# Performance work log

Measured on AMD Instinct MI355X. Metric: run time of the kernel, lower is better.

## Reference

```python
import jax, jax.numpy as jnp
import numpy as np

NUM_HEADS = 16
HEAD_DIM = 64
HIDDEN = NUM_HEADS * HEAD_DIM  # 1024


def get_rel_pos(q_size, k_size, rel_pos):
    # q_size == k_size here and rel_pos already has 2*size-1 rows, so the
    # F.interpolate(mode='linear') resize in the original is an identity.
    # relative_coords = q - k + (k_size - 1)  (scale factors are 1.0)
    coords = jnp.arange(q_size)[:, None] - jnp.arange(k_size)[None, :] + (k_size - 1)
    return rel_pos[coords]  # [q_size, k_size, head_dim]


def setup_inputs() -> dict:
    key = jax.random.key(0)
    ks = jax.random.split(key, 7)
    B, H, W = 4, 56, 28
    inp = {
        "hidden_states": jax.random.normal(ks[0], (B, H, W, HIDDEN), jnp.float32),
        "qkv_w": jax.random.normal(ks[1], (3 * HIDDEN, HIDDEN), jnp.float32) * 0.02,
        "qkv_b": jax.random.normal(ks[2], (3 * HIDDEN,), jnp.float32) * 0.02,
        "proj_w": jax.random.normal(ks[3], (HIDDEN, HIDDEN), jnp.float32) * 0.02,
        "proj_b": jax.random.normal(ks[4], (HIDDEN,), jnp.float32) * 0.02,
        "rel_pos_h": jax.random.normal(ks[5], (2 * H - 1, HEAD_DIM), jnp.float32) * 0.02,
        "rel_pos_w": jax.random.normal(ks[6], (2 * W - 1, HEAD_DIM), jnp.float32) * 0.02,
    }
    return inp


def reference(hidden_states, qkv_w, qkv_b, proj_w, proj_b, rel_pos_h, rel_pos_w):
    B, H, W, C = hidden_states.shape
    N = H * W
    scale = HEAD_DIM ** -0.5

    # qkv projection -> [3, B*heads, N, head_dim]
    qkv = hidden_states @ qkv_w.T + qkv_b
    qkv = qkv.reshape(B, N, 3, NUM_HEADS, HEAD_DIM).transpose(2, 0, 3, 1, 4)
    qkv = qkv.reshape(3, B * NUM_HEADS, N, HEAD_DIM)
    query, key_, value = qkv[0], qkv[1], qkv[2]

    # scaled dot-product scores, fully materialized as in the original
    attn = jnp.einsum('bqd,bkd->bqk', query * scale, key_)  # [B*heads, N, N]

    # decomposed relative position bias
    Rh = get_rel_pos(H, H, rel_pos_h)  # [H, H, d]
    Rw = get_rel_pos(W, W, rel_pos_w)  # [W, W, d]
    q_r = query.reshape(B * NUM_HEADS, H, W, HEAD_DIM)
    rel_h = jnp.einsum('bhwc,hkc->bhwk', q_r, Rh)  # [B*heads, H, W, H]
    rel_w = jnp.einsum('bhwc,wkc->bhwk', q_r, Rw)  # [B*heads, H, W, W]
    attn = attn.reshape(B * NUM_HEADS, H, W, H, W)
    attn = attn + rel_h[:, :, :, :, None] + rel_w[:, :, :, None, :]
    attn = attn.reshape(B * NUM_HEADS, N, N)

    attn = jax.nn.softmax(attn.astype(jnp.float32), axis=-1).astype(query.dtype)

    out = jnp.einsum('bqk,bkd->bqd', attn, value)
    out = out.reshape(B, NUM_HEADS, H, W, HEAD_DIM).transpose(0, 2, 3, 1, 4)
    out = out.reshape(B, H, W, C)
    out = out @ proj_w.T + proj_b
    return out
```

## Files before the change

kernel.cpp:

```cpp
#include <hip/hip_runtime.h>
#include <hip/hip_bf16.h>
#include <stdint.h>

typedef __bf16 bf16;
typedef __bf16 bf16x2 __attribute__((ext_vector_type(2)));
typedef __bf16 bf16x4 __attribute__((ext_vector_type(4)));
typedef __bf16 bf16x8 __attribute__((ext_vector_type(8)));
typedef float f32x4 __attribute__((ext_vector_type(4)));

#define AS1 __attribute__((address_space(1)))
#define AS3 __attribute__((address_space(3)))

static __device__ __forceinline__ void async_cp16(const bf16* g, bf16* l) {
    __builtin_amdgcn_global_load_lds((const AS1 void*)g, (AS3 void*)l, 16, 0, 0);
}

static __device__ __forceinline__ bf16x4 cvt4(f32x4 v) {
    bf16x4 r;
    r[0] = (bf16)v[0]; r[1] = (bf16)v[1]; r[2] = (bf16)v[2]; r[3] = (bf16)v[3];
    return r;
}

static __device__ __forceinline__ float fast_exp2(float x) {
#if __has_builtin(__builtin_amdgcn_exp2f)
    return __builtin_amdgcn_exp2f(x);
#else
    return __expf(x * 0.69314718056f);
#endif
}

__global__ __launch_bounds__(256) void cvt_kernel(
    const float* __restrict__ src, bf16* __restrict__ dst, int n4) {
    int i = blockIdx.x * 256 + threadIdx.x;
    const int stride = gridDim.x * 256;
    for (; i < n4; i += stride)
        ((bf16x4*)dst)[i] = cvt4(((const f32x4*)src)[i]);
}

__global__ __launch_bounds__(256) void build_kone(bf16* __restrict__ Kone) {
    const int idx = blockIdx.x * 256 + threadIdx.x;
    if (idx >= 6400) return;
    const int key = idx >> 2, chunk = idx & 3;
    const int hk = key / 28;
    const int wk = key - hk * 28;
    const int kt = key >> 6;
    const int ha = (kt << 6) / 28;
    const int jw = 27 - wk;
    const int jh = 31 - (hk - ha);
    bf16x8 v;
#pragma unroll
    for (int e = 0; e < 8; e++) {
        const int j = chunk * 8 + e;
        v[e] = (j == jw || j == jh) ? (bf16)1.0f : (bf16)0.0f;
    }
    *(bf16x8*)&Kone[key * 32 + chunk * 8] = v;
}

__global__ __launch_bounds__(256) void zero_slack(
    bf16* __restrict__ a, bf16* __restrict__ b) {
    const int i = threadIdx.x;
    bf16x8 z = {};
    *(bf16x8*)&a[i * 8] = z;
    *(bf16x8*)&b[i * 8] = z;
}


#define QKV_EPILOGUE()                                                        \
    for (int nt = 0; nt < 4; nt++) {                                          \
        const int n_ = n0 + wn + nt * 16 + lm;                                \
        const float bv = bias[n_];                                            \
        const int s = n_ >> 10, rem = n_ & 1023;                              \
        const int h = rem >> 6, d = rem & 63;                                 \
        const float qsc = (s == 0) ? 0.18033688011112042f : 1.0f;             \
        for (int mt = 0; mt < 4; mt++) {                                      \
            for (int r = 0; r < 4; r++) {                                     \
                const int m_ = m0 + wm + mt * 16 + quad * 4 + r;              \
                const int b = m_ / 1568;                                      \
                const int pix = m_ - b * 1568;                                \
                const int g = b * 16 + h;                                     \
                const bf16 v = (bf16)((acc[mt][nt][r] + bv) * qsc);           \
                if (s == 0)      Qb[((size_t)g * 1568 + pix) * 64 + d] = v;   \
                else if (s == 1) Kb[((size_t)g * 1568 + pix) * 64 + d] = v;   \
                else {                                                        \
                    const int lk = pix & 31;                                  \
                    const int ppix = (pix & ~31) | ((lk & 15) << 1) | (lk >> 4); \
                    Vt[((size_t)g * 64 + d) * 1568 + ppix] = v;               \
                }                                                             \
            }                                                                 \
        }                                                                     \
    }


__global__ __launch_bounds__(256) void qkv_gemm_bf16(
    const bf16* __restrict__ A, const bf16* __restrict__ W,
    const float* __restrict__ bias, bf16* __restrict__ Qb,
    bf16* __restrict__ Kb, bf16* __restrict__ Vt) {
    __shared__ bf16 As[128 * 32];
    __shared__ bf16 Bs[128 * 32];
    const int t = threadIdx.x;
    const int wid = t >> 6, lane = t & 63;
    const int bid = blockIdx.x;
    const int widx = (bid & 7) * 147 + (bid >> 3);
    const int mt_ = widx / 24;
    const int m0 = mt_ * 128, n0 = (widx - mt_ * 24) * 128;
    const int wm = (wid & 1) * 64, wn = (wid >> 1) * 64;
    const int r_i = lane >> 2, c8 = (lane & 3) * 8;
    const int lm = lane & 15, quad = lane >> 4;

    f32x4 acc[4][4] = {};
    for (int k0 = 0; k0 < 1024; k0 += 32) {
        __syncthreads();
        for (int i = 0; i < 2; i++) {
            const int blk = wid * 2 + i;
            async_cp16(A + (size_t)(m0 + blk * 16 + r_i) * 1024 + k0 + c8, As + blk * 512);
            async_cp16(W + (size_t)(n0 + blk * 16 + r_i) * 1024 + k0 + c8, Bs + blk * 512);
        }
        __syncthreads();
        bf16x8 af[4], bfr[4];
        for (int x = 0; x < 4; x++) {
            af[x]  = *(const bf16x8*)&As[(wm + x * 16 + lm) * 32 + quad * 8];
            bfr[x] = *(const bf16x8*)&Bs[(wn + x * 16 + lm) * 32 + quad * 8];
        }
        for (int mt = 0; mt < 4; mt++)
            for (int nt = 0; nt < 4; nt++)
                acc[mt][nt] = __builtin_amdgcn_mfma_f32_16x16x32_bf16(af[mt], bfr[nt], acc[mt][nt], 0, 0, 0);
    }
    QKV_EPILOGUE()
}

__global__ __launch_bounds__(256) void qkv_gemm_f32(
    const float* __restrict__ A, const float* __restrict__ W,
    const float* __restrict__ bias, bf16* __restrict__ Qb,
    bf16* __restrict__ Kb, bf16* __restrict__ Vt) {
    __shared__ bf16 As[128 * 32];
    __shared__ bf16 Bs[128 * 32];
    const int t = threadIdx.x;
    const int wid = t >> 6, lane = t & 63;
    const int bid = blockIdx.x;
    const int widx = (bid & 7) * 147 + (bid >> 3);
    const int mt_ = widx / 24;
    const int m0 = mt_ * 128, n0 = (widx - mt_ * 24) * 128;
    const int wm = (wid & 1) * 64, wn = (wid >> 1) * 64;
    const int lm = lane & 15, quad = lane >> 4;

    f32x4 acc[4][4] = {};
    for (int k0 = 0; k0 < 1024; k0 += 32) {
        __syncthreads();
        for (int i = 0; i < 4; i++) {
            const int idx = t + i * 256;
            const int row = idx >> 3, c4 = (idx & 7) * 4;
            const f32x4 av = *(const f32x4*)&A[(size_t)(m0 + row) * 1024 + k0 + c4];
            const f32x4 wv = *(const f32x4*)&W[(size_t)(n0 + row) * 1024 + k0 + c4];
            *(bf16x4*)&As[row * 32 + c4] = cvt4(av);
            *(bf16x4*)&Bs[row * 32 + c4] = cvt4(wv);
        }
        __syncthreads();
        bf16x8 af[4], bfr[4];
        for (int x = 0; x < 4; x++) {
            af[x]  = *(const bf16x8*)&As[(wm + x * 16 + lm) * 32 + quad * 8];
            bfr[x] = *(const bf16x8*)&Bs[(wn + x * 16 + lm) * 32 + quad * 8];
        }
        for (int mt = 0; mt < 4; mt++)
            for (int nt = 0; nt < 4; nt++)
                acc[mt][nt] = __builtin_amdgcn_mfma_f32_16x16x32_bf16(af[mt], bfr[nt], acc[mt][nt], 0, 0, 0);
    }
    QKV_EPILOGUE()
}

__global__ __launch_bounds__(256) void flash_attn(
    const bf16* __restrict__ Qb, const bf16* __restrict__ Kb,
    const bf16* __restrict__ Vt, const float* __restrict__ rph,
    const float* __restrict__ rpw, const bf16* __restrict__ Kone,
    bf16* __restrict__ AO) {
    const int x = blockIdx.x;
    const int xcd = x & 7, j = x >> 3;
    const int g = xcd * 8 + j / 25;
    const int qblk = j - (j / 25) * 25;
    const int q0 = qblk * 64;
    const int hqb = q0 / 28;

    __shared__ __align__(16) char smem[51200];
    bf16* Th = (bf16*)smem;
    const char* ThC = (const char*)smem;
    char* B = smem + 8192;
    bf16* Qs  = (bf16*)(B + 32768);
    bf16* RPh = (bf16*)(B + 0);
    bf16* RPw = (bf16*)(B + 9216);
    float* TwF = (float*)(B + 18432);
    bf16* TwS = (bf16*)(B + 33280);

    const int t = threadIdx.x, wid = t >> 6, lane = t & 63;
    const int lm = lane & 15, quad = lane >> 4;
    const int qbase_l = wid * 16 + quad * 4;
    const int swz = (lm & 7) << 4;
    const int l3 = lane >> 3, l7 = lane & 7;
    const int swe = ((l7 ^ l3) << 3);

    const bf16* kSrc[2];
    const bf16* vSrc[2];
#pragma unroll
    for (int i = 0; i < 2; i++) {
        kSrc[i] = Kb + ((size_t)g * 1568 + wid * 16 + i * 8 + l3) * 64 + swe;
        vSrc[i] = Vt + ((size_t)g * 64 + wid * 16 + i * 8 + l3) * 1568 + swe;
    }

    for (int c = t; c < 512; c += 256) {
        const int row = c >> 3, col = (c & 7) * 8;
        const int qg = min(q0 + row, 1567);
        *(bf16x8*)&Qs[row * 72 + col] =
            *(const bf16x8*)&Qb[((size_t)g * 1568 + qg) * 64 + col];
    }
    for (int c = t; c < 1024; c += 256) {
        const int row = c >> 4, col = (c & 15) * 4;
        const int rg = min(hqb + row, 110);
        *(bf16x4*)&RPh[row * 72 + col] = cvt4(*(const f32x4*)&rph[rg * 64 + col]);
    }
    __syncthreads();

    const int qrow_l = wid * 16 + lm;
    const bf16x8 qf0 = *(const bf16x8*)&Qs[qrow_l * 72 + quad * 8];
    const bf16x8 qf1 = *(const bf16x8*)&Qs[qrow_l * 72 + 32 + quad * 8];
    const int qgl = min(q0 + qrow_l, 1567);
    const int thb2 = (qrow_l * 64 + (qgl / 28 - hqb) + 54) * 2;

    for (int c = t; c < 1024; c += 256) {
        const int row = c >> 4, col = (c & 15) * 4;
        const int rg = min(row, 54);
        *(bf16x4*)&RPw[row * 72 + col] = cvt4(*(const f32x4*)&rpw[rg * 64 + col]);
    }
    f32x4 acch[4];
#pragma unroll
    for (int nt = 0; nt < 4; nt++) {
        const bf16x8 b0 = *(const bf16x8*)&RPh[(nt * 16 + lm) * 72 + quad * 8];
        const bf16x8 b1 = *(const bf16x8*)&RPh[(nt * 16 + lm) * 72 + 32 + quad * 8];
        f32x4 a = {};
        a = __builtin_amdgcn_mfma_f32_16x16x32_bf16(qf0, b0, a, 0, 0, 0);
        a = __builtin_amdgcn_mfma_f32_16x16x32_bf16(qf1, b1, a, 0, 0, 0);
        acch[nt] = a;
    }
    __syncthreads();

#pragma unroll
    for (int nt = 0; nt < 4; nt++) {
        const int c = nt * 16 + lm;
        if (c < 59) {
#pragma unroll
            for (int r = 0; r < 4; r++)
                Th[(qbase_l + r) * 64 + c + 2] = (bf16)(acch[nt][r] * 8.0f);
        }
    }
    if (lm == 0) {
#pragma unroll
        for (int r = 0; r < 4; r++) {
            Th[(qbase_l + r) * 64 + 0] = (bf16)0.0f;
            Th[(qbase_l + r) * 64 + 1] = (bf16)0.0f;
        }
    }
#pragma unroll
    for (int nt = 0; nt < 4; nt++) {
        const bf16x8 b0 = *(const bf16x8*)&RPw[(nt * 16 + lm) * 72 + quad * 8];
        const bf16x8 b1 = *(const bf16x8*)&RPw[(nt * 16 + lm) * 72 + 32 + quad * 8];
        f32x4 a = {};
        a = __builtin_amdgcn_mfma_f32_16x16x32_bf16(qf0, b0, a, 0, 0, 0);
        a = __builtin_amdgcn_mfma_f32_16x16x32_bf16(qf1, b1, a, 0, 0, 0);
        const int c = nt * 16 + lm;
        if (c < 55) {
#pragma unroll
            for (int r = 0; r < 4; r++)
                TwF[(qbase_l + r) * 58 + c] = a[r] * 8.0f;
        }
    }
    __syncthreads();

    {
        const int row = t >> 2, chunk = t & 3;
        const int qg = min(q0 + row, 1567);
        const int wq = qg % 28;
        const float* src = &TwF[row * 58 + wq];
        bf16x8 v;
        if (chunk < 3) {
#pragma unroll
            for (int e = 0; e < 8; e++) v[e] = (bf16)src[chunk * 8 + e];
        } else {
#pragma unroll
            for (int e = 0; e < 4; e++) v[e] = (bf16)src[24 + e];
#pragma unroll
            for (int e = 4; e < 8; e++) v[e] = (bf16)0.0f;
        }
        *(bf16x8*)&TwS[row * 32 + chunk * 8] = v;
    }
    __syncthreads();

    const bf16x8 qt_mine = *(const bf16x8*)&TwS[qrow_l * 32 + quad * 8];

#pragma unroll
    for (int i = 0; i < 2; i++) {
        async_cp16(kSrc[i], (bf16*)(B + (wid * 2 + i) * 1024));
        async_cp16(vSrc[i], (bf16*)(B + 16384 + (wid * 2 + i) * 1024));
        kSrc[i] += 4096;
        vSrc[i] += 64;
    }
    const bf16* kop = Kone + lm * 32 + quad * 8;
    bf16x8 ko[4];
#pragma unroll
    for (int f = 0; f < 4; f++) ko[f] = *(const bf16x8*)(kop + f * 512);
    __syncthreads();

    f32x4 o[4] = {};
    f32x4 lsum = {};
    const f32x4 zero4 = {};
    bf16x8 ones;
#pragma unroll
    for (int i = 0; i < 8; i++) ones[i] = (bf16)1.0f;

    bf16* P0w = (bf16*)(B + 32768) + wid * 640;
    bf16* P1w = (bf16*)(B + 37888) + wid * 640;

    int curo = 0;
    for (int kt = 0; kt < 25; kt++) {
        bf16x8 qf2 = qt_mine;
        if (quad == 3) {
            const int ha = (kt << 6) / 28;
            const char* tp = ThC + (thb2 - (ha << 1));
            qf2[4] = *(const bf16*)(tp);
            qf2[5] = *(const bf16*)(tp + 2);
            qf2[6] = *(const bf16*)(tp + 4);
            qf2[7] = *(const bf16*)(tp + 6);
        }

        if (kt < 24) {
            const int nxto = curo ^ 8192;
#pragma unroll
            for (int i = 0; i < 2; i++) {
                async_cp16(kSrc[i], (bf16*)(B + nxto + (wid * 2 + i) * 1024));
                async_cp16(vSrc[i], (bf16*)(B + 16384 + nxto + (wid * 2 + i) * 1024));
                kSrc[i] += 4096;
                vSrc[i] += 64;
            }
        }

        __builtin_amdgcn_s_setprio(1);
        f32x4 s[4];
#pragma unroll
        for (int f = 0; f < 4; f++)
            s[f] = __builtin_amdgcn_mfma_f32_16x16x32_bf16(qf2, ko[f], zero4, 0, 0, 0);
        {
            const char* KsB = B + curo;
            const int x0 = (quad * 16) ^ swz;
#pragma unroll
            for (int f = 0; f < 4; f++) {
                const char* rp = KsB + (f * 16 + lm) * 128;
                const bf16x8 ka = *(const bf16x8*)(rp + x0);
                const bf16x8 kb2 = *(const bf16x8*)(rp + (x0 ^ 64));
                s[f] = __builtin_amdgcn_mfma_f32_16x16x32_bf16(qf0, ka, s[f], 0, 0, 0);
                s[f] = __builtin_amdgcn_mfma_f32_16x16x32_bf16(qf1, kb2, s[f], 0, 0, 0);
            }
        }
        __builtin_amdgcn_s_setprio(0);

        if (kt < 24) {
            kop += 2048;
#pragma unroll
            for (int f = 0; f < 4; f++) ko[f] = *(const bf16x8*)(kop + f * 512);
        }

        if (kt == 24) {
#pragma unroll
            for (int r = 0; r < 4; r++) { s[2][r] = -30000.0f; s[3][r] = -30000.0f; }
        }

#pragma unroll
        for (int r = 0; r < 4; r++) {
            const float a0 = fast_exp2(s[0][r]);
            const float a1 = fast_exp2(s[1][r]);
            bf16x2 pp; pp[0] = (bf16)a0; pp[1] = (bf16)a1;
            *(bf16x2*)&P0w[(quad * 4 + r) * 40 + lm * 2] = pp;
            const float b0 = fast_exp2(s[2][r]);
            const float b1 = fast_exp2(s[3][r]);
            bf16x2 qq; qq[0] = (bf16)b0; qq[1] = (bf16)b1;
            *(bf16x2*)&P1w[(quad * 4 + r) * 40 + lm * 2] = qq;
        }
        __asm__ volatile("s_waitcnt lgkmcnt(0)" ::: "memory");
        const bf16x8 pf0 = *(const bf16x8*)&P0w[lm * 40 + quad * 8];
        const bf16x8 pf1 = *(const bf16x8*)&P1w[lm * 40 + quad * 8];
        lsum = __builtin_amdgcn_mfma_f32_16x16x32_bf16(pf0, ones, lsum, 0, 0, 0);
        lsum = __builtin_amdgcn_mfma_f32_16x16x32_bf16(pf1, ones, lsum, 0, 0, 0);
        __builtin_amdgcn_s_setprio(1);
        {
            const char* VsB = B + 16384 + curo;
#pragma unroll
            for (int dt = 0; dt < 4; dt++) {
                const bf16x8 vf = *(const bf16x8*)(VsB + (dt * 16 + lm) * 128 +
                                                   ((quad * 16) ^ swz));
                o[dt] = __builtin_amdgcn_mfma_f32_16x16x32_bf16(pf0, vf, o[dt], 0, 0, 0);
            }
#pragma unroll
            for (int dt = 0; dt < 4; dt++) {
                const bf16x8 vf = *(const bf16x8*)(VsB + (dt * 16 + lm) * 128 +
                                                   ((64 + quad * 16) ^ swz));
                o[dt] = __builtin_amdgcn_mfma_f32_16x16x32_bf16(pf1, vf, o[dt], 0, 0, 0);
            }
        }
        __builtin_amdgcn_s_setprio(0);

        if (kt < 24) {
            __syncthreads();
            curo ^= 8192;
        }
    }

    if (q0 + wid * 16 < 1568) {
        const int bo = g >> 4, hh = g & 15;
#pragma unroll
        for (int r = 0; r < 4; r++) {
            const float inv = 1.0f / lsum[r];
            const size_t base = ((size_t)bo * 1568 + q0 + qbase_l + r) * 1024 + hh * 64;
#pragma unroll
            for (int dt = 0; dt < 4; dt++)
                AO[base + dt * 16 + lm] = (bf16)(o[dt][r] * inv);
        }
    }
}

__global__ __launch_bounds__(256) void proj_gemm_bf16(
    const bf16* __restrict__ A, const bf16* __restrict__ W,
    const float* __restrict__ bias, float* __restrict__ out) {
    __shared__ bf16 As[128 * 32];
    __shared__ bf16 Bs[128 * 32];
    const int t = threadIdx.x;
    const int wid = t >> 6, lane = t & 63;
    const int bid = blockIdx.x;
    const int widx = (bid & 7) * 49 + (bid >> 3);
    const int m0 = (widx >> 3) * 128, n0 = (widx & 7) * 128;
    const int wm = (wid & 1) * 64, wn = (wid >> 1) * 64;
    const int r_i = lane >> 2, c8 = (lane & 3) * 8;
    const int lm = lane & 15, quad = lane >> 4;

    f32x4 acc[4][4] = {};
    for (int k0 = 0; k0 < 1024; k0 += 32) {
        __syncthreads();
        for (int i = 0; i < 2; i++) {
            const int blk = wid * 2 + i;
            async_cp16(A + (size_t)(m0 + blk * 16 + r_i) * 1024 + k0 + c8, As + blk * 512);
            async_cp16(W + (size_t)(n0 + blk * 16 + r_i) * 1024 + k0 + c8, Bs + blk * 512);
        }
        __syncthreads();
        bf16x8 af[4], bfr[4];
        for (int x = 0; x < 4; x++) {
            af[x]  = *(const bf16x8*)&As[(wm + x * 16 + lm) * 32 + quad * 8];
            bfr[x] = *(const bf16x8*)&Bs[(wn + x * 16 + lm) * 32 + quad * 8];
        }
        for (int mt = 0; mt < 4; mt++)
            for (int nt = 0; nt < 4; nt++)
                acc[mt][nt] = __builtin_amdgcn_mfma_f32_16x16x32_bf16(af[mt], bfr[nt], acc[mt][nt], 0, 0, 0);
    }
    for (int nt = 0; nt < 4; nt++) {
        const int n_ = n0 + wn + nt * 16 + lm;
        const float bv = bias[n_];
        for (int mt = 0; mt < 4; mt++)
            for (int r = 0; r < 4; r++) {
                const int m_ = m0 + wm + mt * 16 + quad * 4 + r;
                out[(size_t)m_ * 1024 + n_] = acc[mt][nt][r] + bv;
            }
    }
}

__global__ __launch_bounds__(256) void proj_gemm_f32(
    const bf16* __restrict__ A, const float* __restrict__ W,
    const float* __restrict__ bias, float* __restrict__ out) {
    __shared__ bf16 As[128 * 32];
    __shared__ bf16 Bs[128 * 32];
    const int t = threadIdx.x;
    const int wid = t >> 6, lane = t & 63;
    const int bid = blockIdx.x;
    const int widx = (bid & 7) * 49 + (bid >> 3);
    const int m0 = (widx >> 3) * 128, n0 = (widx & 7) * 128;
    const int wm = (wid & 1) * 64, wn = (wid >> 1) * 64;
    const int r_i = lane >> 2, c8 = (lane & 3) * 8;
    const int lm = lane & 15, quad = lane >> 4;

    f32x4 acc[4][4] = {};
    for (int k0 = 0; k0 < 1024; k0 += 32) {
        __syncthreads();
        for (int i = 0; i < 2; i++) {
            const int blk = wid * 2 + i;
            async_cp16(A + (size_t)(m0 + blk * 16 + r_i) * 1024 + k0 + c8, As + blk * 512);
        }
        for (int i = 0; i < 4; i++) {
            const int idx = t + i * 256;
            const int row = idx >> 3, c4 = (idx & 7) * 4;
            const f32x4 wv = *(const f32x4*)&W[(size_t)(n0 + row) * 1024 + k0 + c4];
            *(bf16x4*)&Bs[row * 32 + c4] = cvt4(wv);
        }
        __syncthreads();
        bf16x8 af[4], bfr[4];
        for (int x = 0; x < 4; x++) {
            af[x]  = *(const bf16x8*)&As[(wm + x * 16 + lm) * 32 + quad * 8];
            bfr[x] = *(const bf16x8*)&Bs[(wn + x * 16 + lm) * 32 + quad * 8];
        }
        for (int mt = 0; mt < 4; mt++)
            for (int nt = 0; nt < 4; nt++)
                acc[mt][nt] = __builtin_amdgcn_mfma_f32_16x16x32_bf16(af[mt], bfr[nt], acc[mt][nt], 0, 0, 0);
    }
    for (int nt = 0; nt < 4; nt++) {
        const int n_ = n0 + wn + nt * 16 + lm;
        const float bv = bias[n_];
        for (int mt = 0; mt < 4; mt++)
            for (int r = 0; r < 4; r++) {
                const int m_ = m0 + wm + mt * 16 + quad * 4 + r;
                out[(size_t)m_ * 1024 + n_] = acc[mt][nt][r] + bv;
            }
    }
}

extern "C" void kernel_launch(void* const* d_in, const int* in_sizes, int n_in,
                              void* d_out, int out_size, void* d_ws, size_t ws_size,
                              hipStream_t stream) {
    const float* hs     = (const float*)d_in[0];
    const float* qkv_w  = (const float*)d_in[1];
    const float* qkv_b  = (const float*)d_in[2];
    const float* proj_w = (const float*)d_in[3];
    const float* proj_b = (const float*)d_in[4];
    const float* rph    = (const float*)d_in[5];
    const float* rpw    = (const float*)d_in[6];
    float* out = (float*)d_out;

    const size_t GQ  = (size_t)64 * 1568 * 64;
    const size_t SL  = 2048;
    const size_t N_KONE = (size_t)1600 * 32;
    const size_t N_HS = (size_t)6272 * 1024;
    const size_t N_QW = (size_t)3072 * 1024;
    const size_t N_PW = (size_t)1024 * 1024;
    bf16* Qb = (bf16*)d_ws;
    bf16* Kb = Qb + GQ;
    bf16* Vt = Kb + GQ + SL;
    bf16* AO = Vt + GQ + SL;
    bf16* Kone = AO + GQ;
    bf16* hs_bf    = Kone + N_KONE;
    bf16* qkvw_bf  = hs_bf + N_HS;
    bf16* projw_bf = qkvw_bf + N_QW;
    const size_t need = (4 * GQ + 2 * SL + N_KONE + N_HS + N_QW + N_PW) * sizeof(bf16);

    if (ws_size >= need) {
        build_kone<<<25, 256, 0, stream>>>(Kone);
        zero_slack<<<1, 256, 0, stream>>>(Kb + GQ, Vt + GQ);
        cvt_kernel<<<512, 256, 0, stream>>>(hs, hs_bf, (int)(N_HS / 4));
        cvt_kernel<<<512, 256, 0, stream>>>(qkv_w, qkvw_bf, (int)(N_QW / 4));
        cvt_kernel<<<256, 256, 0, stream>>>(proj_w, projw_bf, (int)(N_PW / 4));
        qkv_gemm_bf16<<<1176, 256, 0, stream>>>(hs_bf, qkvw_bf, qkv_b, Qb, Kb, Vt);
        flash_attn<<<1600, 256, 0, stream>>>(Qb, Kb, Vt, rph, rpw, Kone, AO);
        proj_gemm_bf16<<<392, 256, 0, stream>>>(AO, projw_bf, proj_b, out);
    } else {
        build_kone<<<25, 256, 0, stream>>>(Kone);
        zero_slack<<<1, 256, 0, stream>>>(Kb + GQ, Vt + GQ);
        qkv_gemm_f32<<<1176, 256, 0, stream>>>(hs, qkv_w, qkv_b, Qb, Kb, Vt);
        flash_attn<<<1600, 256, 0, stream>>>(Qb, Kb, Vt, rph, rpw, Kone, AO);
        proj_gemm_f32<<<392, 256, 0, stream>>>(AO, proj_w, proj_b, out);
    }
}
```

Before: 310.1 us.

## Double-buffer GEMM LDS tiles and merge setup/convert kernels into fewer launches

The QKV and projection GEMMs now use two LDS buffers. The next K-slice is prefetched while MFMAs run on the current one, which removes one barrier per iteration and hides global load latency. The three fp32-to-bf16 convert launches are merged into one kernel over a contiguous destination, and the Kone build and slack zeroing are merged into another, cutting launch overhead. Doubling LDS per block to 32KB may lower occupancy. Correctness relies on the hs_bf, qkvw_bf and projw_bf buffers being contiguous in the workspace.

```diff
diff --git a/kernel.cpp b/kernel.cpp
--- a/kernel.cpp
+++ b/kernel.cpp
@@ -29,39 +29,46 @@
 #endif
 }
 
-__global__ __launch_bounds__(256) void cvt_kernel(
-    const float* __restrict__ src, bf16* __restrict__ dst, int n4) {
+__global__ __launch_bounds__(256) void cvt_all(
+    const float* __restrict__ hs, const float* __restrict__ qw,
+    const float* __restrict__ pw, bf16* __restrict__ dst) {
+    const int H4 = 6272 * 1024 / 4, Q4 = 3072 * 1024 / 4, P4 = 1024 * 1024 / 4;
+    const int total = H4 + Q4 + P4;
     int i = blockIdx.x * 256 + threadIdx.x;
     const int stride = gridDim.x * 256;
-    for (; i < n4; i += stride)
-        ((bf16x4*)dst)[i] = cvt4(((const f32x4*)src)[i]);
-}
-
-__global__ __launch_bounds__(256) void build_kone(bf16* __restrict__ Kone) {
+    for (; i < total; i += stride) {
+        f32x4 v;
+        if (i < H4)            v = ((const f32x4*)hs)[i];
+        else if (i < H4 + Q4)  v = ((const f32x4*)qw)[i - H4];
+        else                   v = ((const f32x4*)pw)[i - H4 - Q4];
+        ((bf16x4*)dst)[i] = cvt4(v);
+    }
+}
+
+__global__ __launch_bounds__(256) void setup_misc(
+    bf16* __restrict__ Kone, bf16* __restrict__ slackA, bf16* __restrict__ slackB) {
     const int idx = blockIdx.x * 256 + threadIdx.x;
-    if (idx >= 6400) return;
-    const int key = idx >> 2, chunk = idx & 3;
-    const int hk = key / 28;
-    const int wk = key - hk * 28;
-    const int kt = key >> 6;
-    const int ha = (kt << 6) / 28;
-    const int jw = 27 - wk;
-    const int jh = 31 - (hk - ha);
-    bf16x8 v;
-#pragma unroll
-    for (int e = 0; e < 8; e++) {
-        const int j = chunk * 8 + e;
-        v[e] = (j == jw || j == jh) ? (bf16)1.0f : (bf16)0.0f;
-    }
-    *(bf16x8*)&Kone[key * 32 + chunk * 8] = v;
-}
-
-__global__ __launch_bounds__(256) void zero_slack(
-    bf16* __restrict__ a, bf16* __restrict__ b) {
-    const int i = threadIdx.x;
-    bf16x8 z = {};
-    *(bf16x8*)&a[i * 8] = z;
-    *(bf16x8*)&b[i * 8] = z;
+    if (idx < 6400) {
+        const int key = idx >> 2, chunk = idx & 3;
+        const int hk = key / 28;
+        const int wk = key - hk * 28;
+        const int kt = key >> 6;
+        const int ha = (kt << 6) / 28;
+        const int jw = 27 - wk;
+        const int jh = 31 - (hk - ha);
+        bf16x8 v;
+#pragma unroll
+        for (int e = 0; e < 8; e++) {
+            const int j = chunk * 8 + e;
+            v[e] = (j == jw || j == jh) ? (bf16)1.0f : (bf16)0.0f;
+        }
+        *(bf16x8*)&Kone[key * 32 + chunk * 8] = v;
+    } else if (idx < 6656) {
+        const int i = idx - 6400;
+        bf16x8 z = {};
+        *(bf16x8*)&slackA[i * 8] = z;
+        *(bf16x8*)&slackB[i * 8] = z;
+    }
 }
 
 
@@ -95,8 +102,8 @@
     const bf16* __restrict__ A, const bf16* __restrict__ W,
     const float* __restrict__ bias, bf16* __restrict__ Qb,
     bf16* __restrict__ Kb, bf16* __restrict__ Vt) {
-    __shared__ bf16 As[128 * 32];
-    __shared__ bf16 Bs[128 * 32];
+    __shared__ bf16 As[2][128 * 32];
+    __shared__ bf16 Bs[2][128 * 32];
     const int t = threadIdx.x;
     const int wid = t >> 6, lane = t & 63;
     const int bid = blockIdx.x;
@@ -107,24 +114,33 @@
     const int r_i = lane >> 2, c8 = (lane & 3) * 8;
     const int lm = lane & 15, quad = lane >> 4;
 
+#define QKV_STAGE(buf, kk)                                                     \
+    for (int i = 0; i < 2; i++) {                                              \
+        const int blk = wid * 2 + i;                                           \
+        async_cp16(A + (size_t)(m0 + blk * 16 + r_i) * 1024 + (kk) + c8,       \
+                   &As[buf][blk * 512]);                                       \
+        async_cp16(W + (size_t)(n0 + blk * 16 + r_i) * 1024 + (kk) + c8,       \
+                   &Bs[buf][blk * 512]);                                       \
+    }
+
     f32x4 acc[4][4] = {};
+    QKV_STAGE(0, 0)
+    __syncthreads();
+    int cur = 0;
     for (int k0 = 0; k0 < 1024; k0 += 32) {
-        __syncthreads();
-        for (int i = 0; i < 2; i++) {
-            const int blk = wid * 2 + i;
-            async_cp16(A + (size_t)(m0 + blk * 16 + r_i) * 1024 + k0 + c8, As + blk * 512);
-            async_cp16(W + (size_t)(n0 + blk * 16 + r_i) * 1024 + k0 + c8, Bs + blk * 512);
-        }
-        __syncthreads();
+        if (k0 < 992) { QKV_STAGE(cur ^ 1, k0 + 32) }
         bf16x8 af[4], bfr[4];
         for (int x = 0; x < 4; x++) {
-            af[x]  = *(const bf16x8*)&As[(wm + x * 16 + lm) * 32 + quad * 8];
-            bfr[x] = *(const bf16x8*)&Bs[(wn + x * 16 + lm) * 32 + quad * 8];
+            af[x]  = *(const bf16x8*)&As[cur][(wm + x * 16 + lm) * 32 + quad * 8];
+            bfr[x] = *(const bf16x8*)&Bs[cur][(wn + x * 16 + lm) * 32 + quad * 8];
         }
         for (int mt = 0; mt < 4; mt++)
             for (int nt = 0; nt < 4; nt++)
                 acc[mt][nt] = __builtin_amdgcn_mfma_f32_16x16x32_bf16(af[mt], bfr[nt], acc[mt][nt], 0, 0, 0);
-    }
+        __syncthreads();
+        cur ^= 1;
+    }
+#undef QKV_STAGE
     QKV_EPILOGUE()
 }
 
@@ -132,8 +148,8 @@
     const float* __restrict__ A, const float* __restrict__ W,
     const float* __restrict__ bias, bf16* __restrict__ Qb,
     bf16* __restrict__ Kb, bf16* __restrict__ Vt) {
-    __shared__ bf16 As[128 * 32];
-    __shared__ bf16 Bs[128 * 32];
+    __shared__ bf16 As[2][128 * 32];
+    __shared__ bf16 Bs[2][128 * 32];
     const int t = threadIdx.x;
     const int wid = t >> 6, lane = t & 63;
     const int bid = blockIdx.x;
@@ -143,27 +159,34 @@
     const int wm = (wid & 1) * 64, wn = (wid >> 1) * 64;
     const int lm = lane & 15, quad = lane >> 4;
 
+#define QKVF_STAGE(buf, kk)                                                    \
+    for (int i = 0; i < 4; i++) {                                              \
+        const int idx = t + i * 256;                                           \
+        const int row = idx >> 3, c4 = (idx & 7) * 4;                          \
+        const f32x4 av = *(const f32x4*)&A[(size_t)(m0 + row) * 1024 + (kk) + c4]; \
+        const f32x4 wv = *(const f32x4*)&W[(size_t)(n0 + row) * 1024 + (kk) + c4]; \
+        *(bf16x4*)&As[buf][row * 32 + c4] = cvt4(av);                          \
+        *(bf16x4*)&Bs[buf][row * 32 + c4] = cvt4(wv);                          \
+    }
+
     f32x4 acc[4][4] = {};
+    QKVF_STAGE(0, 0)
+    __syncthreads();
+    int cur = 0;
     for (int k0 = 0; k0 < 1024; k0 += 32) {
-        __syncthreads();
-        for (int i = 0; i < 4; i++) {
-            const int idx = t + i * 256;
-            const int row = idx >> 3, c4 = (idx & 7) * 4;
-            const f32x4 av = *(const f32x4*)&A[(size_t)(m0 + row) * 1024 + k0 + c4];
-            const f32x4 wv = *(const f32x4*)&W[(size_t)(n0 + row) * 1024 + k0 + c4];
-            *(bf16x4*)&As[row * 32 + c4] = cvt4(av);
-            *(bf16x4*)&Bs[row * 32 + c4] = cvt4(wv);
-        }
-        __syncthreads();
+        if (k0 < 992) { QKVF_STAGE(cur ^ 1, k0 + 32) }
         bf16x8 af[4], bfr[4];
         for (int x = 0; x < 4; x++) {
-            af[x]  = *(const bf16x8*)&As[(wm + x * 16 + lm) * 32 + quad * 8];
-            bfr[x] = *(const bf16x8*)&Bs[(wn + x * 16 + lm) * 32 + quad * 8];
+            af[x]  = *(const bf16x8*)&As[cur][(wm + x * 16 + lm) * 32 + quad * 8];
+            bfr[x] = *(const bf16x8*)&Bs[cur][(wn + x * 16 + lm) * 32 + quad * 8];
         }
         for (int mt = 0; mt < 4; mt++)
             for (int nt = 0; nt < 4; nt++)
                 acc[mt][nt] = __builtin_amdgcn_mfma_f32_16x16x32_bf16(af[mt], bfr[nt], acc[mt][nt], 0, 0, 0);
-    }
+        __syncthreads();
+        cur ^= 1;
+    }
+#undef QKVF_STAGE
     QKV_EPILOGUE()
 }
 
@@ -425,8 +448,8 @@
 __global__ __launch_bounds__(256) void proj_gemm_bf16(
     const bf16* __restrict__ A, const bf16* __restrict__ W,
     const float* __restrict__ bias, float* __restrict__ out) {
-    __shared__ bf16 As[128 * 32];
-    __shared__ bf16 Bs[128 * 32];
+    __shared__ bf16 As[2][128 * 32];
+    __shared__ bf16 Bs[2][128 * 32];
     const int t = threadIdx.x;
     const int wid = t >> 6, lane = t & 63;
     const int bid = blockIdx.x;
@@ -436,24 +459,33 @@
     const int r_i = lane >> 2, c8 = (lane & 3) * 8;
     const int lm = lane & 15, quad = lane >> 4;
 
+#define PROJ_STAGE(buf, kk)                                                    \
+    for (int i = 0; i < 2; i++) {                                              \
+        const int blk = wid * 2 + i;                                           \
+        async_cp16(A + (size_t)(m0 + blk * 16 + r_i) * 1024 + (kk) + c8,       \
+                   &As[buf][blk * 512]);                                       \
+        async_cp16(W + (size_t)(n0 + blk * 16 + r_i) * 1024 + (kk) + c8,       \
+                   &Bs[buf][blk * 512]);                                       \
+    }
+
     f32x4 acc[4][4] = {};
+    PROJ_STAGE(0, 0)
+    __syncthreads();
+    int cur = 0;
     for (int k0 = 0; k0 < 1024; k0 += 32) {
-        __syncthreads();
-        for (int i = 0; i < 2; i++) {
-            const int blk = wid * 2 + i;
-            async_cp16(A + (size_t)(m0 + blk * 16 + r_i) * 1024 + k0 + c8, As + blk * 512);
-            async_cp16(W + (size_t)(n0 + blk * 16 + r_i) * 1024 + k0 + c8, Bs + blk * 512);
-        }
-        __syncthreads();
+        if (k0 < 992) { PROJ_STAGE(cur ^ 1, k0 + 32) }
         bf16x8 af[4], bfr[4];
         for (int x = 0; x < 4; x++) {
-            af[x]  = *(const bf16x8*)&As[(wm + x * 16 + lm) * 32 + quad * 8];
-            bfr[x] = *(const bf16x8*)&Bs[(wn + x * 16 + lm) * 32 + quad * 8];
+            af[x]  = *(const bf16x8*)&As[cur][(wm + x * 16 + lm) * 32 + quad * 8];
+            bfr[x] = *(const bf16x8*)&Bs[cur][(wn + x * 16 + lm) * 32 + quad * 8];
         }
         for (int mt = 0; mt < 4; mt++)
             for (int nt = 0; nt < 4; nt++)
                 acc[mt][nt] = __builtin_amdgcn_mfma_f32_16x16x32_bf16(af[mt], bfr[nt], acc[mt][nt], 0, 0, 0);
-    }
+        __syncthreads();
+        cur ^= 1;
+    }
+#undef PROJ_STAGE
     for (int nt = 0; nt < 4; nt++) {
         const int n_ = n0 + wn + nt * 16 + lm;
         const float bv = bias[n_];
@@ -468,8 +500,8 @@
 __global__ __launch_bounds__(256) void proj_gemm_f32(
     const bf16* __restrict__ A, const float* __restrict__ W,
     const float* __restrict__ bias, float* __restrict__ out) {
-    __shared__ bf16 As[128 * 32];
-    __shared__ bf16 Bs[128 * 32];
+    __shared__ bf16 As[2][128 * 32];
+    __shared__ bf16 Bs[2][128 * 32];
     const int t = threadIdx.x;
     const int wid = t >> 6, lane = t & 63;
     const int bid = blockIdx.x;
@@ -479,29 +511,37 @@
     const int r_i = lane >> 2, c8 = (lane & 3) * 8;
     const int lm = lane & 15, quad = lane >> 4;
 
+#define PROJF_STAGE(buf, kk)                                                   \
+    for (int i = 0; i < 2; i++) {                                              \
+        const int blk = wid * 2 + i;                                           \
+        async_cp16(A + (size_t)(m0 + blk * 16 + r_i) * 1024 + (kk) + c8,       \
+                   &As[buf][blk * 512]);                                       \
+    }                                                                          \
+    for (int i = 0; i < 4; i++) {                                              \
+        const int idx = t + i * 256;                                           \
+        const int row = idx >> 3, c4 = (idx & 7) * 4;                          \
+        const f32x4 wv = *(const f32x4*)&W[(size_t)(n0 + row) * 1024 + (kk) + c4]; \
+        *(bf16x4*)&Bs[buf][row * 32 + c4] = cvt4(wv);                          \
+    }
+
     f32x4 acc[4][4] = {};
+    PROJF_STAGE(0, 0)
+    __syncthreads();
+    int cur = 0;
     for (int k0 = 0; k0 < 1024; k0 += 32) {
-        __syncthreads();
-        for (int i = 0; i < 2; i++) {
-            const int blk = wid * 2 + i;
-            async_cp16(A + (size_t)(m0 + blk * 16 + r_i) * 1024 + k0 + c8, As + blk * 512);
-        }
-        for (int i = 0; i < 4; i++) {
-            const int idx = t + i * 256;
-            const int row = idx >> 3, c4 = (idx & 7) * 4;
-            const f32x4 wv = *(const f32x4*)&W[(size_t)(n0 + row) * 1024 + k0 + c4];
-            *(bf16x4*)&Bs[row * 32 + c4] = cvt4(wv);
-        }
-        __syncthreads();
+        if (k0 < 992) { PROJF_STAGE(cur ^ 1, k0 + 32) }
         bf16x8 af[4], bfr[4];
         for (int x = 0; x < 4; x++) {
-            af[x]  = *(const bf16x8*)&As[(wm + x * 16 + lm) * 32 + quad * 8];
-            bfr[x] = *(const bf16x8*)&Bs[(wn + x * 16 + lm) * 32 + quad * 8];
+            af[x]  = *(const bf16x8*)&As[cur][(wm + x * 16 + lm) * 32 + quad * 8];
+            bfr[x] = *(const bf16x8*)&Bs[cur][(wn + x * 16 + lm) * 32 + quad * 8];
         }
         for (int mt = 0; mt < 4; mt++)
             for (int nt = 0; nt < 4; nt++)
                 acc[mt][nt] = __builtin_amdgcn_mfma_f32_16x16x32_bf16(af[mt], bfr[nt], acc[mt][nt], 0, 0, 0);
-    }
+        __syncthreads();
+        cur ^= 1;
+    }
+#undef PROJF_STAGE
     for (int nt = 0; nt < 4; nt++) {
         const int n_ = n0 + wn + nt * 16 + lm;
         const float bv = bias[n_];
@@ -542,17 +582,13 @@
     const size_t need = (4 * GQ + 2 * SL + N_KONE + N_HS + N_QW + N_PW) * sizeof(bf16);
 
     if (ws_size >= need) {
-        build_kone<<<25, 256, 0, stream>>>(Kone);
-        zero_slack<<<1, 256, 0, stream>>>(Kb + GQ, Vt + GQ);
-        cvt_kernel<<<512, 256, 0, stream>>>(hs, hs_bf, (int)(N_HS / 4));
-        cvt_kernel<<<512, 256, 0, stream>>>(qkv_w, qkvw_bf, (int)(N_QW / 4));
-        cvt_kernel<<<256, 256, 0, stream>>>(proj_w, projw_bf, (int)(N_PW / 4));
+        setup_misc<<<26, 256, 0, stream>>>(Kone, Kb + GQ, Vt + GQ);
+        cvt_all<<<1024, 256, 0, stream>>>(hs, qkv_w, proj_w, hs_bf);
         qkv_gemm_bf16<<<1176, 256, 0, stream>>>(hs_bf, qkvw_bf, qkv_b, Qb, Kb, Vt);
         flash_attn<<<1600, 256, 0, stream>>>(Qb, Kb, Vt, rph, rpw, Kone, AO);
         proj_gemm_bf16<<<392, 256, 0, stream>>>(AO, projw_bf, proj_b, out);
     } else {
-        build_kone<<<25, 256, 0, stream>>>(Kone);
-        zero_slack<<<1, 256, 0, stream>>>(Kb + GQ, Vt + GQ);
+        setup_misc<<<26, 256, 0, stream>>>(Kone, Kb + GQ, Vt + GQ);
         qkv_gemm_f32<<<1176, 256, 0, stream>>>(hs, qkv_w, qkv_b, Qb, Kb, Vt);
         flash_attn<<<1600, 256, 0, stream>>>(Qb, Kb, Vt, rph, rpw, Kone, AO);
         proj_gemm_f32<<<392, 256, 0, stream>>>(AO, proj_w, proj_b, out);
```

Result: faster. 294.9 us (-4.9%).
